# Optimization experiments

Measured on AMD Instinct MI355X. Metric: run time of the kernel, lower is better.

## Reference

```python
import jax, jax.numpy as jnp
import numpy as np

A, H, HI = 4, 3, 2  # nagents, n_pol_heads, n_intr_rew_heads (sep_extr_head=True)
# leave-one-out index table: row i lists all agents k != i, in ascending order (torch loop order)
LOO = np.array([[k for k in range(A) if k != i] for i in range(A)])  # [A, A-1]


def setup_inputs() -> dict:
    key = jax.random.key(0)
    ks = jax.random.split(key, 12)
    B, S, C, D = 32768, 256, 16, 128  # batch, vect_state_size, action_size, hidden_dim
    IN = C * (A - 1) + D  # 176 critic input dim
    r = lambda k, shp, s=0.05: jax.random.normal(k, shp, dtype=jnp.float32) * s
    return {
        "state_vect": jax.random.normal(ks[0], (B, S), dtype=jnp.float32),
        "acs": jax.random.normal(ks[1], (A, H, B, C), dtype=jnp.float32),
        "enc_W": r(ks[2], (S, D)),
        "enc_b": r(ks[3], (D,)),
        "extr_W1": r(ks[4], (H, A, IN, D)),
        "extr_b1": r(ks[5], (H, A, D)),
        "extr_W2": r(ks[6], (H, A, D, C)),
        "extr_b2": r(ks[7], (H, A, C)),
        "intr_W1": r(ks[8], (HI, A, IN, D)),
        "intr_b1": r(ks[9], (HI, A, D)),
        "intr_W2": r(ks[10], (HI, A, D, C)),
        "intr_b2": r(ks[11], (HI, A, C)),
    }


def reference(state_vect, acs, enc_W, enc_b, extr_W1, extr_b1, extr_W2, extr_b2,
              intr_W1, intr_b1, intr_W2, intr_b2):
    B, C = acs.shape[2], acs.shape[3]
    D = enc_W.shape[1]
    # shared state encoder: Linear -> ReLU
    enc = jax.nn.relu(state_vect @ enc_W + enc_b)  # [B, D]
    # leave-one-out action concat per (agent, head): cat(acs[k!=i, j]) ++ enc
    rel = acs[LOO]                                 # [A, A-1, H, B, C]
    rel = rel.transpose(0, 2, 3, 1, 4).reshape(A, H, B, (A - 1) * C)
    x = jnp.concatenate([rel, jnp.broadcast_to(enc, (A, H, B, D))], axis=-1)  # [A,H,B,IN]
    # greedy action index of agent i's own head-j policy output
    int_acs = jnp.argmax(acs, axis=-1)             # [A, H, B]

    def critic(xin, W1, b1, W2, b2):
        # xin: [A, Hc, B, IN]; W1: [Hc, A, IN, D]; W2: [Hc, A, D, C]
        h = jax.nn.relu(jnp.einsum('ahbi,haid->ahbd', xin, W1)
                        + b1.transpose(1, 0, 2)[:, :, None, :])
        return (jnp.einsum('ahbd,hadc->ahbc', h, W2)
                + b2.transpose(1, 0, 2)[:, :, None, :])  # [A, Hc, B, C]

    extr_all_q = critic(x, extr_W1, extr_b1, extr_W2, extr_b2)          # [A,H,B,C]
    extr_q = jnp.take_along_axis(extr_all_q, int_acs[..., None], axis=-1)  # [A,H,B,1]
    # intr critics exist only for heads j>=1 (sep_extr_head=True -> offset -1)
    intr_all_q = critic(x[:, 1:], intr_W1, intr_b1, intr_W2, intr_b2)   # [A,HI,B,C]
    intr_q = jnp.take_along_axis(intr_all_q, int_acs[:, 1:, :, None], axis=-1)  # [A,HI,B,1]
    return extr_q, intr_q
```

## Files before the change

kernel.cpp:

```cpp
#include <hip/hip_runtime.h>

#define NA 4
#define NH 3
#define NHI 2
#define Bsz 32768
#define Ssz 256
#define Csz 16
#define Dsz 128
#define INsz 176
#define NP 20
#define KP 192

typedef __bf16 v8bf __attribute__((ext_vector_type(8)));
typedef float v4f __attribute__((ext_vector_type(4)));

#define OFF_ENC    0
#define OFF_ACSBF  8388608
#define OFF_W1F    20971520
#define OFF_W2T    22020096
#define OFF_AMX    22102016
#define OFF_ZERO   22495232

#define N_ACSROW (NA*NH*Bsz)
#define N_W1F   (NP*192*32)
#define N_W2T   (NP*Csz*Dsz)
#define N_ZERO  16
#define N_PREP  (N_ACSROW+N_W1F+N_W2T+N_ZERO)
#define ENC_BLOCKS (Bsz / 64)
#define PREP_BLOCKS ((N_PREP + 255) / 256)

__global__ __launch_bounds__(256) void pe_kernel(
    const float* __restrict__ sv, const float* __restrict__ encb,
    const float* __restrict__ acs, const float* __restrict__ encW,
    const float* __restrict__ eW1, const float* __restrict__ iW1,
    const float* __restrict__ eW2, const float* __restrict__ iW2,
    char* __restrict__ ws)
{
    __shared__ __bf16 encs[8 * 8 * 512];
    const int t = threadIdx.x;

    if (blockIdx.x < ENC_BLOCKS) {
        #pragma unroll
        for (int i = 0; i < 16; ++i) {
            const int slot = i * 256 + t;
            const int kcnt = slot >> 6;
            const int ln   = slot & 63;
            const int kc = kcnt >> 3, nt = kcnt & 7;
            const int qq = ln >> 4, mm = ln & 15;
            const int krow = kc * 32 + qq * 8;
            const int col  = nt * 16 + mm;
            v8bf o;
            #pragma unroll
            for (int j = 0; j < 8; ++j)
                o[j] = (__bf16)encW[(size_t)(krow + j) * Dsz + col];
            *(v8bf*)&encs[(size_t)kcnt * 512 + ln * 8] = o;
        }
        __syncthreads();

        const int wv = t >> 6, lane = t & 63, m = lane & 15, q = lane >> 4;
        const int R = blockIdx.x * 64 + wv * 16 + m;
        __bf16* enc = (__bf16*)(ws + OFF_ENC);

        v4f acc[8];
        #pragma unroll
        for (int nt = 0; nt < 8; ++nt) acc[nt] = (v4f){0.f, 0.f, 0.f, 0.f};

        const float* arow = sv + (size_t)R * Ssz + q * 8;
        #pragma unroll
        for (int kc = 0; kc < 8; ++kc) {
            float4 f0 = *(const float4*)(arow + kc * 32);
            float4 f1 = *(const float4*)(arow + kc * 32 + 4);
            v8bf af;
            af[0]=(__bf16)f0.x; af[1]=(__bf16)f0.y; af[2]=(__bf16)f0.z; af[3]=(__bf16)f0.w;
            af[4]=(__bf16)f1.x; af[5]=(__bf16)f1.y; af[6]=(__bf16)f1.z; af[7]=(__bf16)f1.w;
            #pragma unroll
            for (int nt = 0; nt < 8; ++nt) {
                v8bf bf = *(const v8bf*)&encs[((size_t)kc * 8 + nt) * 512 + lane * 8];
                acc[nt] = __builtin_amdgcn_mfma_f32_16x16x32_bf16(af, bf, acc[nt], 0, 0, 0);
            }
        }
        const int rbase = blockIdx.x * 64 + wv * 16 + q * 4;
        #pragma unroll
        for (int nt = 0; nt < 8; ++nt) {
            const float bias = encb[nt * 16 + m];
            #pragma unroll
            for (int rg = 0; rg < 4; ++rg) {
                float v = acc[nt][rg] + bias;
                v = v > 0.f ? v : 0.f;
                enc[(size_t)(rbase + rg) * Dsz + nt * 16 + m] = (__bf16)v;
            }
        }
        return;
    }

    long tid = (long)(blockIdx.x - ENC_BLOCKS) * 256 + t;

    if (tid < N_ACSROW) {
        const float4* src = (const float4*)(acs + (size_t)tid * 16);
        float4 f0 = src[0], f1 = src[1], f2 = src[2], f3 = src[3];
        float v[16] = {f0.x,f0.y,f0.z,f0.w, f1.x,f1.y,f1.z,f1.w,
                       f2.x,f2.y,f2.z,f2.w, f3.x,f3.y,f3.z,f3.w};
        v8bf o0, o1;
        #pragma unroll
        for (int i = 0; i < 8; ++i) { o0[i] = (__bf16)v[i]; o1[i] = (__bf16)v[8 + i]; }
        v8bf* dst = (v8bf*)(ws + OFF_ACSBF) + tid * 2;
        dst[0] = o0; dst[1] = o1;
        float best = v[0]; int bi = 0;
        #pragma unroll
        for (int c = 1; c < 16; ++c) if (v[c] > best) { best = v[c]; bi = c; }
        ((unsigned char*)(ws + OFF_AMX))[tid] = (unsigned char)bi;
        return;
    }
    tid -= N_ACSROW;
    if (tid < N_W1F) {
        const int n4 = (int)(tid & 31) * 4;
        const int k  = (int)((tid >> 5) % 192);
        const int p  = (int)(tid / 6144);
        const float* W1;
        if (p < 12) { int ai = p / 3, hj = p % 3; W1 = eW1 + (size_t)(hj * NA + ai) * INsz * Dsz; }
        else { int qq = p - 12; int ai = qq >> 1, jj = qq & 1; W1 = iW1 + (size_t)(jj * NA + ai) * INsz * Dsz; }
        float4 f = (k < INsz) ? *(const float4*)(W1 + (size_t)k * Dsz + n4)
                              : (float4){0.f, 0.f, 0.f, 0.f};
        const int kc = k >> 5, q = (k >> 3) & 3, j = k & 7;
        __bf16* dst = (__bf16*)(ws + OFF_W1F);
        const float fv[4] = {f.x, f.y, f.z, f.w};
        #pragma unroll
        for (int i = 0; i < 4; ++i) {
            const int n = n4 + i, nt = n >> 4, m = n & 15;
            dst[((size_t)(p * 6 + kc) * 8 + nt) * 512 + (q * 16 + m) * 8 + j] = (__bf16)fv[i];
        }
        return;
    }
    tid -= N_W1F;
    if (tid < N_W2T) {
        int d = (int)(tid & 127);
        int rest = (int)(tid >> 7);
        int c = rest & 15, p = rest >> 4;
        const float* W2;
        if (p < 12) { int ai = p / 3, hj = p % 3; W2 = eW2 + (size_t)(hj * NA + ai) * Dsz * Csz; }
        else { int qq = p - 12; int ai = qq >> 1, jj = qq & 1; W2 = iW2 + (size_t)(jj * NA + ai) * Dsz * Csz; }
        ((__bf16*)(ws + OFF_W2T))[(size_t)p * Csz * Dsz + (size_t)c * Dsz + d] = (__bf16)W2[(size_t)d * Csz + c];
        return;
    }
    tid -= N_W2T;
    if (tid < N_ZERO) ((float*)(ws + OFF_ZERO))[tid] = 0.f;
}

__global__ __launch_bounds__(256, 2) void critic_kernel(
    const float* __restrict__ eb1, const float* __restrict__ eb2,
    const float* __restrict__ ib1, const float* __restrict__ ib2,
    const char* __restrict__ ws, float* __restrict__ out)
{
    __shared__ __bf16 w1s[6 * 8 * 512];

    const int t = threadIdx.x;
    const int p  = blockIdx.y;
    const int rb = blockIdx.x;
    const int wv = t >> 6, lane = t & 63, m = lane & 15, q = lane >> 4;
    const int rw = rb * 256 + wv * 64;

    int ai, hj;
    const float *b1, *b2;
    float* outp;
    if (p < 12) {
        ai = p / 3; hj = p % 3;
        const int wi = hj * NA + ai;
        b1 = eb1 + (size_t)wi * Dsz; b2 = eb2 + (size_t)wi * Csz;
        outp = out + (size_t)(ai * NH + hj) * Bsz;
    } else {
        const int qq = p - 12; ai = qq >> 1; const int jj = qq & 1; hj = jj + 1;
        const int wi = jj * NA + ai;
        b1 = ib1 + (size_t)wi * Dsz; b2 = ib2 + (size_t)wi * Csz;
        outp = out + (size_t)NA * NH * Bsz + (size_t)(ai * NHI + jj) * Bsz;
    }

    const __bf16* acsb = (const __bf16*)(ws + OFF_ACSBF);
    const __bf16* encp = (const __bf16*)(ws + OFF_ENC);
    const __bf16* w1f  = (const __bf16*)(ws + OFF_W1F) + (size_t)p * 6 * 8 * 512;
    const __bf16* w2t  = (const __bf16*)(ws + OFF_W2T) + (size_t)p * Csz * Dsz;
    const unsigned char* amx = (const unsigned char*)(ws + OFF_AMX) + (size_t)(ai * NH + hj) * Bsz + rw;
    const __bf16* zerop = (const __bf16*)(ws + OFF_ZERO);

    {
        const v8bf* src = (const v8bf*)w1f;
        v8bf* dst = (v8bf*)w1s;
        #pragma unroll
        for (int i = 0; i < 12; ++i)
            dst[i * 256 + t] = src[i * 256 + t];
    }

    const int loo0 = 0 + (0 >= ai), loo1 = 1 + (1 >= ai), loo2 = 2 + (2 >= ai);
    const __bf16* a0p = acsb + (size_t)(loo0 * NH + hj) * Bsz * Csz;
    const __bf16* a1p = acsb + (size_t)(loo1 * NH + hj) * Bsz * Csz;
    const __bf16* a2p = acsb + (size_t)(loo2 * NH + hj) * Bsz * Csz;

    const int R0 = rw + m;
    const __bf16* base[6];
    int strd[6];
    base[0] = (q < 2) ? (a0p + (size_t)R0 * Csz + q * 8) : (a1p + (size_t)R0 * Csz + (q - 2) * 8);
    strd[0] = Csz;
    base[1] = (q < 2) ? (a2p + (size_t)R0 * Csz + q * 8) : (encp + (size_t)R0 * Dsz + (q - 2) * 8);
    strd[1] = (q < 2) ? Csz : Dsz;
    base[2] = encp + (size_t)R0 * Dsz + 16 + q * 8;  strd[2] = Dsz;
    base[3] = encp + (size_t)R0 * Dsz + 48 + q * 8;  strd[3] = Dsz;
    base[4] = encp + (size_t)R0 * Dsz + 80 + q * 8;  strd[4] = Dsz;
    base[5] = (q < 2) ? (encp + (size_t)R0 * Dsz + 112 + q * 8) : zerop;
    strd[5] = (q < 2) ? Dsz : 0;

    v4f acc[4][8];
    #pragma unroll
    for (int i = 0; i < 4; ++i)
        #pragma unroll
        for (int j = 0; j < 8; ++j)
            acc[i][j] = (v4f){0.f, 0.f, 0.f, 0.f};

    __syncthreads();

    #pragma unroll
    for (int kc = 0; kc < 6; ++kc) {
        v8bf af[4];
        #pragma unroll
        for (int mt = 0; mt < 4; ++mt)
            af[mt] = *(const v8bf*)(base[kc] + (size_t)(mt * 16) * strd[kc]);
        #pragma unroll
        for (int nt = 0; nt < 8; ++nt) {
            v8bf bf = *(const v8bf*)&w1s[((size_t)kc * 8 + nt) * 512 + lane * 8];
            #pragma unroll
            for (int mt = 0; mt < 4; ++mt)
                acc[mt][nt] = __builtin_amdgcn_mfma_f32_16x16x32_bf16(af[mt], bf, acc[mt][nt], 0, 0, 0);
        }
    }

    float b1v[8];
    #pragma unroll
    for (int nt = 0; nt < 8; ++nt) b1v[nt] = b1[nt * 16 + m];

    #pragma unroll
    for (int mt = 0; mt < 4; ++mt) {
        const int rowb = mt * 16 + q * 4;
        const unsigned int cw = *(const unsigned int*)(amx + rowb);
        #pragma unroll
        for (int rg = 0; rg < 4; ++rg) {
            const int c = (cw >> (8 * rg)) & 255;
            const __bf16* wc = w2t + (size_t)c * Dsz + m;
            float partial = 0.f;
            #pragma unroll
            for (int nt = 0; nt < 8; ++nt) {
                float h = acc[mt][nt][rg] + b1v[nt];
                h = h > 0.f ? h : 0.f;
                partial += h * (float)wc[nt * 16];
            }
            partial += __shfl_xor(partial, 1, 64);
            partial += __shfl_xor(partial, 2, 64);
            partial += __shfl_xor(partial, 4, 64);
            partial += __shfl_xor(partial, 8, 64);
            if (m == 0)
                outp[rw + rowb + rg] = partial + b2[c];
        }
    }
}

extern "C" void kernel_launch(void* const* d_in, const int* in_sizes, int n_in,
                              void* d_out, int out_size, void* d_ws, size_t ws_size,
                              hipStream_t stream) {
    const float* sv   = (const float*)d_in[0];
    const float* acs  = (const float*)d_in[1];
    const float* encW = (const float*)d_in[2];
    const float* encb = (const float*)d_in[3];
    const float* eW1  = (const float*)d_in[4];
    const float* eb1  = (const float*)d_in[5];
    const float* eW2  = (const float*)d_in[6];
    const float* eb2  = (const float*)d_in[7];
    const float* iW1  = (const float*)d_in[8];
    const float* ib1  = (const float*)d_in[9];
    const float* iW2  = (const float*)d_in[10];
    const float* ib2  = (const float*)d_in[11];
    float* out = (float*)d_out;
    char* ws = (char*)d_ws;

    hipLaunchKernelGGL(pe_kernel, dim3(ENC_BLOCKS + PREP_BLOCKS), dim3(256), 0, stream,
                       sv, encb, acs, encW, eW1, iW1, eW2, iW2, ws);
    hipLaunchKernelGGL(critic_kernel, dim3(Bsz / 256, NP), dim3(256), 0, stream,
                       eb1, eb2, ib1, ib2, ws, out);
}
```

Before: 183.9 us.

## Switch critic GEMM to 32x32x16 MFMA with exact K=176 and LDS-staged W2

Rewrites the critic layer-1 GEMM to use 32x32x16 bf16 MFMA tiles over K=176 in 11 steps instead of 16x16x32 with K padded to 192. This removes the padding work and the zero buffer. The W1 prepack layout changes to match, and W2, b1 and b2 are staged into LDS for the gather-dot epilogue. Each block now covers 128 rows, so the grid doubles, and launch bounds allow 3 blocks per CU. The cost is a longer shuffle reduction over 32 lanes and a different register footprint.

After: 181.6 us. No clear change (-1.3%).

```diff
diff --git a/kernel.cpp b/kernel.cpp
--- a/kernel.cpp
+++ b/kernel.cpp
@@ -9,23 +9,21 @@
 #define Dsz 128
 #define INsz 176
 #define NP 20
-#define KP 192
 
 typedef __bf16 v8bf __attribute__((ext_vector_type(8)));
 typedef float v4f __attribute__((ext_vector_type(4)));
+typedef float v16f __attribute__((ext_vector_type(16)));
 
 #define OFF_ENC    0
 #define OFF_ACSBF  8388608
 #define OFF_W1F    20971520
 #define OFF_W2T    22020096
 #define OFF_AMX    22102016
-#define OFF_ZERO   22495232
 
 #define N_ACSROW (NA*NH*Bsz)
-#define N_W1F   (NP*192*32)
+#define N_W1F   (NP*176*32)
 #define N_W2T   (NP*Csz*Dsz)
-#define N_ZERO  16
-#define N_PREP  (N_ACSROW+N_W1F+N_W2T+N_ZERO)
+#define N_PREP  (N_ACSROW+N_W1F+N_W2T)
 #define ENC_BLOCKS (Bsz / 64)
 #define PREP_BLOCKS ((N_PREP + 255) / 256)
 
@@ -114,20 +112,19 @@
     tid -= N_ACSROW;
     if (tid < N_W1F) {
         const int n4 = (int)(tid & 31) * 4;
-        const int k  = (int)((tid >> 5) % 192);
-        const int p  = (int)(tid / 6144);
+        const int k  = (int)((tid >> 5) % 176);
+        const int p  = (int)(tid / 5632);
         const float* W1;
         if (p < 12) { int ai = p / 3, hj = p % 3; W1 = eW1 + (size_t)(hj * NA + ai) * INsz * Dsz; }
         else { int qq = p - 12; int ai = qq >> 1, jj = qq & 1; W1 = iW1 + (size_t)(jj * NA + ai) * INsz * Dsz; }
-        float4 f = (k < INsz) ? *(const float4*)(W1 + (size_t)k * Dsz + n4)
-                              : (float4){0.f, 0.f, 0.f, 0.f};
-        const int kc = k >> 5, q = (k >> 3) & 3, j = k & 7;
-        __bf16* dst = (__bf16*)(ws + OFF_W1F);
+        float4 f = *(const float4*)(W1 + (size_t)k * Dsz + n4);
+        const int s = k >> 4, half = (k >> 3) & 1, j = k & 7;
+        __bf16* dst = (__bf16*)(ws + OFF_W1F) + (size_t)p * 22528;
         const float fv[4] = {f.x, f.y, f.z, f.w};
         #pragma unroll
         for (int i = 0; i < 4; ++i) {
-            const int n = n4 + i, nt = n >> 4, m = n & 15;
-            dst[((size_t)(p * 6 + kc) * 8 + nt) * 512 + (q * 16 + m) * 8 + j] = (__bf16)fv[i];
+            const int n = n4 + i, nt = n >> 5, ln = half * 32 + (n & 31);
+            dst[((size_t)(s * 4 + nt) * 64 + ln) * 8 + j] = (__bf16)fv[i];
         }
         return;
     }
@@ -142,22 +139,24 @@
         ((__bf16*)(ws + OFF_W2T))[(size_t)p * Csz * Dsz + (size_t)c * Dsz + d] = (__bf16)W2[(size_t)d * Csz + c];
         return;
     }
-    tid -= N_W2T;
-    if (tid < N_ZERO) ((float*)(ws + OFF_ZERO))[tid] = 0.f;
 }
 
-__global__ __launch_bounds__(256, 2) void critic_kernel(
+__global__ __launch_bounds__(256, 3) void critic_kernel(
     const float* __restrict__ eb1, const float* __restrict__ eb2,
     const float* __restrict__ ib1, const float* __restrict__ ib2,
     const char* __restrict__ ws, float* __restrict__ out)
 {
-    __shared__ __bf16 w1s[6 * 8 * 512];
+    __shared__ __bf16 w1s[11 * 4 * 512];
+    __shared__ __bf16 w2s[16 * 136];
+    __shared__ float  b1s[128];
+    __shared__ float  b2s[16];
 
     const int t = threadIdx.x;
     const int p  = blockIdx.y;
     const int rb = blockIdx.x;
-    const int wv = t >> 6, lane = t & 63, m = lane & 15, q = lane >> 4;
-    const int rw = rb * 256 + wv * 64;
+    const int wv = t >> 6, lane = t & 63;
+    const int col = lane & 31, half = lane >> 5;
+    const int rw = rb * 128 + wv * 32;
 
     int ai, hj;
     const float *b1, *b2;
@@ -176,17 +175,20 @@
 
     const __bf16* acsb = (const __bf16*)(ws + OFF_ACSBF);
     const __bf16* encp = (const __bf16*)(ws + OFF_ENC);
-    const __bf16* w1f  = (const __bf16*)(ws + OFF_W1F) + (size_t)p * 6 * 8 * 512;
+    const __bf16* w1f  = (const __bf16*)(ws + OFF_W1F) + (size_t)p * 22528;
     const __bf16* w2t  = (const __bf16*)(ws + OFF_W2T) + (size_t)p * Csz * Dsz;
     const unsigned char* amx = (const unsigned char*)(ws + OFF_AMX) + (size_t)(ai * NH + hj) * Bsz + rw;
-    const __bf16* zerop = (const __bf16*)(ws + OFF_ZERO);
 
     {
         const v8bf* src = (const v8bf*)w1f;
         v8bf* dst = (v8bf*)w1s;
         #pragma unroll
-        for (int i = 0; i < 12; ++i)
+        for (int i = 0; i < 11; ++i)
             dst[i * 256 + t] = src[i * 256 + t];
+        const int c = t >> 4, d = (t & 15) * 8;
+        *(v8bf*)&w2s[c * 136 + d] = *(const v8bf*)(w2t + c * 128 + d);
+        if (t < 128) b1s[t] = b1[t];
+        if (t < 16)  b2s[t] = b2[t];
     }
 
     const int loo0 = 0 + (0 >= ai), loo1 = 1 + (1 >= ai), loo2 = 2 + (2 >= ai);
@@ -194,69 +196,63 @@
     const __bf16* a1p = acsb + (size_t)(loo1 * NH + hj) * Bsz * Csz;
     const __bf16* a2p = acsb + (size_t)(loo2 * NH + hj) * Bsz * Csz;
 
-    const int R0 = rw + m;
-    const __bf16* base[6];
-    int strd[6];
-    base[0] = (q < 2) ? (a0p + (size_t)R0 * Csz + q * 8) : (a1p + (size_t)R0 * Csz + (q - 2) * 8);
-    strd[0] = Csz;
-    base[1] = (q < 2) ? (a2p + (size_t)R0 * Csz + q * 8) : (encp + (size_t)R0 * Dsz + (q - 2) * 8);
-    strd[1] = (q < 2) ? Csz : Dsz;
-    base[2] = encp + (size_t)R0 * Dsz + 16 + q * 8;  strd[2] = Dsz;
-    base[3] = encp + (size_t)R0 * Dsz + 48 + q * 8;  strd[3] = Dsz;
-    base[4] = encp + (size_t)R0 * Dsz + 80 + q * 8;  strd[4] = Dsz;
-    base[5] = (q < 2) ? (encp + (size_t)R0 * Dsz + 112 + q * 8) : zerop;
-    strd[5] = (q < 2) ? Dsz : 0;
-
-    v4f acc[4][8];
-    #pragma unroll
-    for (int i = 0; i < 4; ++i)
-        #pragma unroll
-        for (int j = 0; j < 8; ++j)
-            acc[i][j] = (v4f){0.f, 0.f, 0.f, 0.f};
+    const int R = rw + col;
+    v8bf af[11];
+    af[0] = *(const v8bf*)(a0p + (size_t)R * Csz + half * 8);
+    af[1] = *(const v8bf*)(a1p + (size_t)R * Csz + half * 8);
+    af[2] = *(const v8bf*)(a2p + (size_t)R * Csz + half * 8);
+    #pragma unroll
+    for (int s = 3; s < 11; ++s)
+        af[s] = *(const v8bf*)(encp + (size_t)R * Dsz + (s - 3) * 16 + half * 8);
+
+    unsigned int cwv[8];
+    #pragma unroll
+    for (int i = 0; i < 8; ++i)
+        cwv[i] = *(const unsigned int*)(amx + i * 4);
+    unsigned int cwsel[4];
+    #pragma unroll
+    for (int rr = 0; rr < 4; ++rr)
+        cwsel[rr] = half ? cwv[rr * 2 + 1] : cwv[rr * 2];
+
+    v16f acc[4];
+    #pragma unroll
+    for (int nt = 0; nt < 4; ++nt)
+        #pragma unroll
+        for (int i = 0; i < 16; ++i) acc[nt][i] = 0.f;
 
     __syncthreads();
 
     #pragma unroll
-    for (int kc = 0; kc < 6; ++kc) {
-        v8bf af[4];
-        #pragma unroll
-        for (int mt = 0; mt < 4; ++mt)
-            af[mt] = *(const v8bf*)(base[kc] + (size_t)(mt * 16) * strd[kc]);
-        #pragma unroll
-        for (int nt = 0; nt < 8; ++nt) {
-            v8bf bf = *(const v8bf*)&w1s[((size_t)kc * 8 + nt) * 512 + lane * 8];
-            #pragma unroll
-            for (int mt = 0; mt < 4; ++mt)
-                acc[mt][nt] = __builtin_amdgcn_mfma_f32_16x16x32_bf16(af[mt], bf, acc[mt][nt], 0, 0, 0);
-        }
-    }
-
-    float b1v[8];
-    #pragma unroll
-    for (int nt = 0; nt < 8; ++nt) b1v[nt] = b1[nt * 16 + m];
-
-    #pragma unroll
-    for (int mt = 0; mt < 4; ++mt) {
-        const int rowb = mt * 16 + q * 4;
-        const unsigned int cw = *(const unsigned int*)(amx + rowb);
-        #pragma unroll
-        for (int rg = 0; rg < 4; ++rg) {
-            const int c = (cw >> (8 * rg)) & 255;
-            const __bf16* wc = w2t + (size_t)c * Dsz + m;
-            float partial = 0.f;
-            #pragma unroll
-            for (int nt = 0; nt < 8; ++nt) {
-                float h = acc[mt][nt][rg] + b1v[nt];
-                h = h > 0.f ? h : 0.f;
-                partial += h * (float)wc[nt * 16];
-            }
-            partial += __shfl_xor(partial, 1, 64);
-            partial += __shfl_xor(partial, 2, 64);
-            partial += __shfl_xor(partial, 4, 64);
-            partial += __shfl_xor(partial, 8, 64);
-            if (m == 0)
-                outp[rw + rowb + rg] = partial + b2[c];
-        }
+    for (int s = 0; s < 11; ++s) {
+        #pragma unroll
+        for (int nt = 0; nt < 4; ++nt) {
+            v8bf bf = *(const v8bf*)&w1s[((size_t)(s * 4 + nt)) * 512 + lane * 8];
+            acc[nt] = __builtin_amdgcn_mfma_f32_32x32x16_bf16(af[s], bf, acc[nt], 0, 0, 0);
+        }
+    }
+
+    float b1v[4];
+    #pragma unroll
+    for (int nt = 0; nt < 4; ++nt) b1v[nt] = b1s[nt * 32 + col];
+
+    #pragma unroll
+    for (int reg = 0; reg < 16; ++reg) {
+        const int rr = reg >> 2, r4 = reg & 3;
+        const int c = (cwsel[rr] >> (r4 * 8)) & 255;
+        float partial = 0.f;
+        #pragma unroll
+        for (int nt = 0; nt < 4; ++nt) {
+            float h = acc[nt][reg] + b1v[nt];
+            h = h > 0.f ? h : 0.f;
+            partial += h * (float)w2s[c * 136 + nt * 32 + col];
+        }
+        partial += __shfl_xor(partial, 1, 64);
+        partial += __shfl_xor(partial, 2, 64);
+        partial += __shfl_xor(partial, 4, 64);
+        partial += __shfl_xor(partial, 8, 64);
+        partial += __shfl_xor(partial, 16, 64);
+        if (col == 0)
+            outp[rw + r4 + 8 * rr + 4 * half] = partial + b2s[c];
     }
 }
 
@@ -280,6 +276,6 @@
 
     hipLaunchKernelGGL(pe_kernel, dim3(ENC_BLOCKS + PREP_BLOCKS), dim3(256), 0, stream,
                        sv, encb, acs, encW, eW1, iW1, eW2, iW2, ws);
-    hipLaunchKernelGGL(critic_kernel, dim3(Bsz / 256, NP), dim3(256), 0, stream,
+    hipLaunchKernelGGL(critic_kernel, dim3(Bsz / 128, NP), dim3(256), 0, stream,
                        eb1, eb2, ib1, ib2, ws, out);
 }
```
